# Kernel tuning notes

Hardware: AMD Instinct MI355X
Metric: run time of the kernel (lower is better)

Reference implementation:

```python
import math
import jax, jax.numpy as jnp
import numpy as np

B, T, D = 2, 1024, 768          # batch, seq, hidden
H = 12                          # attention heads
DH_ATT = D // H
PH, NK, TOPK, DHK = 4, 256, 32, 128  # pkm heads, num product keys, topk, key dim
DQ = PH * DHK * 2               # pkm query projection width
EPS = 1e-5


def _ln(x, g, b):
    m = jnp.mean(x, -1, keepdims=True)
    v = jnp.var(x, -1, keepdims=True)
    return (x - m) * jax.lax.rsqrt(v + EPS) * g + b


def setup_inputs() -> dict:
    key = jax.random.key(0)
    k = jax.random.split(key, 8)
    n = lambda i, s, sc=0.02: jax.random.normal(k[i], s, jnp.float32) * sc
    z = lambda s: jnp.zeros(s, jnp.float32)
    o = lambda s: jnp.ones(s, jnp.float32)
    return {
        "hidden_states": jax.random.normal(k[0], (B, T, D), jnp.float32),
        "wq": n(1, (D, D)), "bq": z((D,)),
        "wk": n(2, (D, D)), "bk": z((D,)),
        "wv": n(3, (D, D)), "bv": z((D,)),
        "wo": n(4, (D, D)), "bo": z((D,)),
        "ln1_g": o((D,)), "ln1_b": z((D,)),
        "ln2_g": o((D,)), "ln2_b": z((D,)),
        "pkm_wq": n(5, (D, DQ)),
        "bn_g": o((DQ,)), "bn_b": z((DQ,)),
        "pkm_keys": n(6, (PH, NK, 2, DHK), 1.0 / math.sqrt(DHK)),
        "pkm_values": n(7, (NK * NK, D), 1.0 / math.sqrt(D)),
    }


def reference(hidden_states, wq, bq, wk, bk, wv, bv, wo, bo,
              ln1_g, ln1_b, ln2_g, ln2_b,
              pkm_wq, bn_g, bn_b, pkm_keys, pkm_values):
    x = hidden_states
    # ---- pre-norm self-attention + residual ----
    h = _ln(x, ln1_g, ln1_b)
    q = (h @ wq + bq).reshape(B, T, H, DH_ATT)
    k = (h @ wk + bk).reshape(B, T, H, DH_ATT)
    v = (h @ wv + bv).reshape(B, T, H, DH_ATT)
    scores = jnp.einsum('bqhd,bkhd->bhqk', q, k) / math.sqrt(DH_ATT)
    probs = jax.nn.softmax(scores, axis=-1)
    attn_out = jnp.einsum('bhqk,bkhd->bqhd', probs, v).reshape(B, T, D) @ wo + bo
    x = x + attn_out
    # ---- pre-norm PKM + residual ----
    h = _ln(x, ln2_g, ln2_b)
    qf = (h @ pkm_wq).reshape(B * T, DQ)
    # BatchNorm1d over tokens (training-mode batch stats)
    mu = jnp.mean(qf, 0)
    var = jnp.var(qf, 0)
    qn = (qf - mu) * jax.lax.rsqrt(var + EPS) * bn_g + bn_b
    # split into the two sub-key query halves: [2, n, PH, DHK]
    qh = jnp.stack(jnp.split(qn, 2, axis=-1)).reshape(2, B * T, PH, DHK)
    # distances against both sub-key codebooks: [n, PH, 2, NK]
    dots = jnp.einsum('pnhd,hkpd->nhpk', qh, pkm_keys)
    s, idx = jax.lax.top_k(dots, TOPK)                       # [n, PH, 2, TOPK]
    all_s = (s[:, :, 0, :, None] + s[:, :, 1, None, :]).reshape(B * T, PH, TOPK * TOPK)
    all_i = (idx[:, :, 0, :, None] * NK + idx[:, :, 1, None, :]).reshape(B * T, PH, TOPK * TOPK)
    fs, fpos = jax.lax.top_k(all_s, TOPK)                    # [n, PH, TOPK]
    vi = jnp.take_along_axis(all_i, fpos, axis=-1)           # cartesian indices
    attn = jax.nn.softmax(fs, axis=-1)
    # EmbeddingBag(mode='sum') with per_sample_weights: gather + weighted sum over PH*TOPK
    pkm_out = jnp.einsum('nhk,nhkd->nd', attn, pkm_values[vi]).reshape(B, T, D)
    return x + pkm_out
```

## Files before the change

kernel.cpp:

```cpp
#include <hip/hip_runtime.h>
#include <hip/hip_bf16.h>

#define B_  2
#define T_  1024
#define D_  768
#define H_  12
#define NT  2048
#define DQ_ 1024
#define PH_ 4
#define NK_ 256
#define TK_ 32
#define DHK_ 128
#define QKVLD 2304
#define CVHALF 25165824L
#define NKEYS (PH_ * NK_ * 2 * DHK_)
#define PREPBLKS 3584

typedef __attribute__((ext_vector_type(8))) short bf16x8;
typedef __attribute__((ext_vector_type(4))) float f32x4;
typedef __attribute__((ext_vector_type(2))) float f32x2;

static __device__ __forceinline__ unsigned short f2bf(float f) {
    union { float f; unsigned u; } c; c.f = f;
    unsigned r = (c.u + 0x7fffu + ((c.u >> 16) & 1u)) >> 16;
    return (unsigned short)r;
}

static __device__ __forceinline__ float bf2f(unsigned short s) {
    union { unsigned u; float f; } c; c.u = ((unsigned)s) << 16;
    return c.f;
}

__device__ __constant__ unsigned short ctab[128] = {
    0,1,2,3,4,5,6,7,8,9,10,11,12,13,14,15,16,17,18,19,20,21,22,23,24,25,26,27,28,29,30,31,
    32,33,34,35,36,37,38,39,40,41,42,43,44,45,46,47,
    64,65,66,67,68,69,70,71,72,73,
    96,97,98,99,100,101,102,103,
    128,129,130,131,132,133,
    160,161,162,163,164,
    192,193,194,195,
    224,225,226,227,
    256,257,258,
    288,289,290,
    320,321, 352,353, 384,385, 416,417, 448,449, 480,481,
    512,544,576,608,640,672,704,736,768,800,832,864,896,928,960,992,
    0xFFFF,0xFFFF,0xFFFF,0xFFFF,0xFFFF,0xFFFF,0xFFFF,0xFFFF,0xFFFF
};

__global__ __launch_bounds__(256)
void ln_kernel(const float* __restrict__ x, const float* __restrict__ g,
               const float* __restrict__ b, unsigned short* __restrict__ out,
               int nrows,
               const float* __restrict__ wq, const float* __restrict__ wk,
               const float* __restrict__ wv, const float* __restrict__ wo,
               const float* __restrict__ pwq, const float* __restrict__ keys,
               unsigned short* __restrict__ wqkvT, unsigned short* __restrict__ woT,
               unsigned short* __restrict__ pwqT, unsigned short* __restrict__ keyB) {
    int tid = threadIdx.x;
    if ((int)blockIdx.x >= nrows) {
        int tb = blockIdx.x - nrows;
        if (tb >= 3072) {
            long i = ((long)(tb - 3072) * 256 + tid) * 2;
            if (i + 1 < NKEYS + 1) { keyB[i] = f2bf(keys[i]); keyB[i + 1] = f2bf(keys[i + 1]); }
            return;
        }
        __shared__ float t[32][33];
        const float* W; unsigned short* Wt; int N, kx, ny;
        if (tb < 2304) {
            int z = tb / 576, rem = tb % 576;
            kx = rem % 24; ny = rem / 24; N = 768;
            if (z == 0)      { W = wq; Wt = wqkvT; }
            else if (z == 1) { W = wk; Wt = wqkvT + 589824; }
            else if (z == 2) { W = wv; Wt = wqkvT + 2 * 589824; }
            else             { W = wo; Wt = woT; }
        } else {
            int rem = tb - 2304;
            kx = rem % 24; ny = rem / 24; N = 1024;
            W = pwq; Wt = pwqT;
        }
        int k0 = kx * 32, n0 = ny * 32;
        int tx = tid & 31, ty = tid >> 5;
#pragma unroll
        for (int i = 0; i < 4; ++i)
            t[ty + 8 * i][tx] = W[(long)(k0 + ty + 8 * i) * N + n0 + tx];
        __syncthreads();
#pragma unroll
        for (int i = 0; i < 4; ++i)
            Wt[(long)(n0 + ty + 8 * i) * 768 + k0 + tx] = f2bf(t[tx][ty + 8 * i]);
        return;
    }

    int row = blockIdx.x;
    const float* xr = x + (long)row * D_;
    float v0 = xr[tid], v1 = xr[tid + 256], v2 = xr[tid + 512];
    float s = v0 + v1 + v2, ss = v0 * v0 + v1 * v1 + v2 * v2;
#pragma unroll
    for (int o = 1; o < 64; o <<= 1) { s += __shfl_xor(s, o); ss += __shfl_xor(ss, o); }
    __shared__ float ps[4], pss[4];
    int wid = tid >> 6, lane = tid & 63;
    if (lane == 0) { ps[wid] = s; pss[wid] = ss; }
    __syncthreads();
    s = ps[0] + ps[1] + ps[2] + ps[3];
    ss = pss[0] + pss[1] + pss[2] + pss[3];
    float mean = s * (1.f / D_);
    float var = ss * (1.f / D_) - mean * mean;
    float rs = rsqrtf(var + 1e-5f);
    unsigned short* orow = out + (long)row * D_;
    orow[tid]       = f2bf((v0 - mean) * rs * g[tid]       + b[tid]);
    orow[tid + 256] = f2bf((v1 - mean) * rs * g[tid + 256] + b[tid + 256]);
    orow[tid + 512] = f2bf((v2 - mean) * rs * g[tid + 512] + b[tid + 512]);
}

__global__ __launch_bounds__(256)
void gemm_kernel(const unsigned short* __restrict__ A, int lda,
                 const unsigned short* __restrict__ Bt, int ldb,
                 const float* __restrict__ bias,
                 const float* __restrict__ bias2,
                 const float* __restrict__ bias3,
                 const float* __restrict__ res,
                 float* __restrict__ outF,
                 unsigned short* __restrict__ outB,
                 int ldc, int K, int zmode,
                 const float* __restrict__ cvin,
                 unsigned char* __restrict__ cvout,
                 long cvbase, int cvy0,
                 float* __restrict__ pSo, float* __restrict__ pSSo) {
    if (cvin && (int)blockIdx.y >= cvy0) {
        long stride = (long)(gridDim.y - cvy0) * gridDim.x * 256 * 8;
        long idx = cvbase +
            ((long)((blockIdx.y - cvy0) * gridDim.x + blockIdx.x) * 256 + threadIdx.x) * 8;
        long end = cvbase + CVHALF;
#pragma unroll 2
        for (; idx < end; idx += stride) {
            f32x4 a = *(const f32x4*)(cvin + idx);
            f32x4 b = *(const f32x4*)(cvin + idx + 4);
            int lo = __builtin_amdgcn_cvt_pk_fp8_f32(a[0], a[1], 0, false);
            lo = __builtin_amdgcn_cvt_pk_fp8_f32(a[2], a[3], lo, true);
            int hi = __builtin_amdgcn_cvt_pk_fp8_f32(b[0], b[1], 0, false);
            hi = __builtin_amdgcn_cvt_pk_fp8_f32(b[2], b[3], hi, true);
            *(uint2*)(cvout + idx) = make_uint2((unsigned)lo, (unsigned)hi);
        }
        return;
    }
    const int tid = threadIdx.x;
    const int w = tid >> 6, lane = tid & 63;
    const int ls = lane & 15, g = lane >> 4;
    const int m0 = blockIdx.x * 64, n0 = blockIdx.y * 64;

    __shared__ unsigned short As[64][40];
    __shared__ unsigned short Bs[64][40];

    f32x4 acc[4];
#pragma unroll
    for (int c = 0; c < 4; ++c) acc[c] = (f32x4){0.f, 0.f, 0.f, 0.f};

    const int lrow = tid >> 2, lseg = tid & 3;
    const unsigned short* gA = A + (long)(m0 + lrow) * lda + lseg * 8;
    const unsigned short* gB = Bt + (long)(n0 + lrow) * ldb + lseg * 8;

    for (int kt = 0; kt < K; kt += 32) {
        __syncthreads();
        *(int4*)&As[lrow][lseg * 8] = *(const int4*)(gA + kt);
        *(int4*)&Bs[lrow][lseg * 8] = *(const int4*)(gB + kt);
        __syncthreads();
        bf16x8 bfr = *(const bf16x8*)&Bs[w * 16 + ls][g * 8];
#pragma unroll
        for (int c = 0; c < 4; ++c) {
            bf16x8 afr = *(const bf16x8*)&As[c * 16 + ls][g * 8];
            acc[c] = __builtin_amdgcn_mfma_f32_16x16x32_bf16(afr, bfr, acc[c], 0, 0, 0);
        }
    }
#pragma unroll
    for (int c = 0; c < 4; ++c) {
#pragma unroll
        for (int r = 0; r < 4; ++r) {
            int row = m0 + c * 16 + g * 4 + r;
            int col = n0 + w * 16 + ls;
            float v = acc[c][r];
            if (bias) {
                const float* bp = bias; int cc = col;
                if (zmode == 2) {
                    int sel = col >= 1536 ? 2 : (col >= 768 ? 1 : 0);
                    bp = sel == 0 ? bias : (sel == 1 ? bias2 : bias3);
                    cc = col - sel * 768;
                }
                v += bp[cc];
            }
            long off = (long)row * ldc + col;
            if (res)  v += res[off];
            if (outF) outF[off] = v;
            if (outB) outB[off] = f2bf(v);
        }
    }
    if (pSo) {
        float s = 0.f, ss = 0.f;
#pragma unroll
        for (int c = 0; c < 4; ++c)
#pragma unroll
            for (int r = 0; r < 4; ++r) { float v = acc[c][r]; s += v; ss += v * v; }
        s += __shfl_xor(s, 16); s += __shfl_xor(s, 32);
        ss += __shfl_xor(ss, 16); ss += __shfl_xor(ss, 32);
        if (g == 0) {
            int col = n0 + w * 16 + ls;
            pSo[(long)blockIdx.x * DQ_ + col] = s;
            pSSo[(long)blockIdx.x * DQ_ + col] = ss;
        }
    }
}

__global__ __launch_bounds__(256)
void dots_kernel(const unsigned short* __restrict__ qf,
                 const unsigned short* __restrict__ Bt,
                 const float* __restrict__ pS, const float* __restrict__ pSS,
                 const float* __restrict__ bng, const float* __restrict__ bnb,
                 unsigned short* __restrict__ outB) {
    int z = blockIdx.z, ph = z >> 1, half = z & 1;
    const int cbase = half * 512 + ph * 128;
    const unsigned short* A = qf + cbase;
    Bt   += ph * 65536 + half * 128;
    outB += ph * 512 + half * 256;
    const int tid = threadIdx.x;
    const int w = tid >> 6, lane = tid & 63;
    const int ls = lane & 15, g = lane >> 4;
    const int m0 = blockIdx.x * 64, n0 = blockIdx.y * 64;

    __shared__ unsigned short As[64][136];
    __shared__ unsigned short Bs[64][136];
    __shared__ float ggs[128], bbs[128];

    const int row = tid >> 2, cs = (tid & 3) * 32;
    const unsigned short* gA = A + (long)(m0 + row) * DQ_ + cs;
    const unsigned short* gB = Bt + (long)(n0 + row) * 256 + cs;

    bf16x8 areg[4];
#pragma unroll
    for (int j = 0; j < 4; ++j) {
        areg[j] = *(const bf16x8*)(gA + 8 * j);
        *(int4*)&Bs[row][cs + 8 * j] = *(const int4*)(gB + 8 * j);
    }
    if (tid < 128) {
        int c = cbase + tid;
        float s = 0.f, ss = 0.f;
#pragma unroll 8
        for (int i = 0; i < 32; ++i) { s += pS[(long)i * DQ_ + c]; ss += pSS[(long)i * DQ_ + c]; }
        float m = s * (1.f / NT);
        float rs = rsqrtf(ss * (1.f / NT) - m * m + 1e-5f);
        float gg = bng[c] * rs;
        ggs[tid] = gg;
        bbs[tid] = bnb[c] - m * gg;
    }
    __syncthreads();
#pragma unroll
    for (int j = 0; j < 4; ++j) {
        bf16x8 r;
#pragma unroll
        for (int k = 0; k < 8; ++k) {
            int lc = cs + 8 * j + k;
            r[k] = (short)f2bf(bf2f((unsigned short)areg[j][k]) * ggs[lc] + bbs[lc]);
        }
        *(bf16x8*)&As[row][cs + 8 * j] = r;
    }
    __syncthreads();

    f32x4 acc[4];
#pragma unroll
    for (int c = 0; c < 4; ++c) acc[c] = (f32x4){0.f, 0.f, 0.f, 0.f};
#pragma unroll
    for (int kk = 0; kk < 4; ++kk) {
        bf16x8 bfr = *(const bf16x8*)&Bs[w * 16 + ls][g * 8 + 32 * kk];
#pragma unroll
        for (int c = 0; c < 4; ++c) {
            bf16x8 afr = *(const bf16x8*)&As[c * 16 + ls][g * 8 + 32 * kk];
            acc[c] = __builtin_amdgcn_mfma_f32_16x16x32_bf16(afr, bfr, acc[c], 0, 0, 0);
        }
    }
#pragma unroll
    for (int c = 0; c < 4; ++c)
#pragma unroll
        for (int r = 0; r < 4; ++r)
            outB[(long)(m0 + c * 16 + g * 4 + r) * 2048 + n0 + w * 16 + ls] = f2bf(acc[c][r]);
}

__global__ __launch_bounds__(512)
void attn_mfma_kernel(const unsigned short* __restrict__ qkv,
                      unsigned short* __restrict__ outg) {
    int bh = blockIdx.x, bb = bh / H_, hh = bh % H_;
    int q0 = blockIdx.y * 128;
    int tid = threadIdx.x, wv = tid >> 6, lane = tid & 63;
    int ls = lane & 15, g = lane >> 4;

    __shared__ unsigned short Klds[128 * 64];
    __shared__ unsigned short Vlds[64 * 128];
    __shared__ unsigned short Plds[8][16 * 128];

    const unsigned short* qrow = qkv + (long)(bb * T_ + q0 + wv * 16 + ls) * QKVLD + hh * 64 + g * 8;
    bf16x8 qf0 = *(const bf16x8*)qrow;
    bf16x8 qf1 = *(const bf16x8*)(qrow + 32);

    f32x4 o_acc[4];
#pragma unroll
    for (int nf = 0; nf < 4; ++nf) o_acc[nf] = (f32x4){0.f, 0.f, 0.f, 0.f};
    float mrun[4] = {-1e30f, -1e30f, -1e30f, -1e30f};
    float lrun[4] = {0.f, 0.f, 0.f, 0.f};

    char* pbase = (char*)&Plds[wv][0];
    const bool doK = tid < 256;
    const int t2 = tid & 255;
    const int d0 = (t2 & 7) * 8, kvq = t2 >> 3;

    bf16x8 streg[4];
    auto loadKV = [&](int kvb) {
        if (doK) {
#pragma unroll
            for (int i = 0; i < 4; ++i) {
                int c = t2 + i * 256;
                streg[i] = *(const bf16x8*)(qkv + (long)(bb * T_ + kvb + (c >> 3)) * QKVLD + 768 + hh * 64 + (c & 7) * 8);
            }
        } else {
            const unsigned short* vb = qkv + (long)(bb * T_ + kvb + kvq * 4) * QKVLD + 1536 + hh * 64 + d0;
#pragma unroll
            for (int i = 0; i < 4; ++i) streg[i] = *(const bf16x8*)(vb + i * QKVLD);
        }
    };

    loadKV(0);
    for (int kt = 0; kt < T_ / 128; ++kt) {
        __syncthreads();
        if (doK) {
#pragma unroll
            for (int i = 0; i < 4; ++i) {
                int c = t2 + i * 256;
                int kv = c >> 3, dc = c & 7;
                *(bf16x8*)((char*)Klds + ((kv * 128 + dc * 16) ^ ((kv & 7) << 4))) = streg[i];
            }
        } else {
#pragma unroll
            for (int j = 0; j < 8; ++j) {
                unsigned lo = (unsigned)(unsigned short)streg[0][j] | ((unsigned)(unsigned short)streg[1][j] << 16);
                unsigned hi = (unsigned)(unsigned short)streg[2][j] | ((unsigned)(unsigned short)streg[3][j] << 16);
                int d = d0 + j;
                *(uint2*)((char*)Vlds + ((d * 256 + kvq * 8) ^ ((d & 7) << 4))) = make_uint2(lo, hi);
            }
        }
        __syncthreads();
        if (kt + 1 < T_ / 128) loadKV((kt + 1) * 128);

        f32x4 sa[8];
#pragma unroll
        for (int f = 0; f < 8; ++f) sa[f] = (f32x4){0.f, 0.f, 0.f, 0.f};
        __builtin_amdgcn_s_setprio(1);
#pragma unroll
        for (int f = 0; f < 8; ++f) {
            int kv = f * 16 + ls;
            bf16x8 b0 = *(const bf16x8*)((char*)Klds + ((kv * 128 + g * 16) ^ ((kv & 7) << 4)));
            bf16x8 b1 = *(const bf16x8*)((char*)Klds + ((kv * 128 + 64 + g * 16) ^ ((kv & 7) << 4)));
            sa[f] = __builtin_amdgcn_mfma_f32_16x16x32_bf16(qf0, b0, sa[f], 0, 0, 0);
            sa[f] = __builtin_amdgcn_mfma_f32_16x16x32_bf16(qf1, b1, sa[f], 0, 0, 0);
        }
        __builtin_amdgcn_s_setprio(0);

        float pw[8][4];
#pragma unroll
        for (int f = 0; f < 8; ++f)
#pragma unroll
            for (int r = 0; r < 4; ++r) pw[f][r] = sa[f][r] * 0.125f;
#pragma unroll
        for (int r = 0; r < 4; ++r) {
            float m = pw[0][r];
#pragma unroll
            for (int f = 1; f < 8; ++f) m = fmaxf(m, pw[f][r]);
            m = fmaxf(m, __shfl_xor(m, 1));
            m = fmaxf(m, __shfl_xor(m, 2));
            m = fmaxf(m, __shfl_xor(m, 4));
            m = fmaxf(m, __shfl_xor(m, 8));
            if (m > mrun[r] + 8.f) {
                float fac = __expf(mrun[r] - m);
                lrun[r] *= fac;
#pragma unroll
                for (int nf = 0; nf < 4; ++nf) o_acc[nf][r] *= fac;
                mrun[r] = m;
            }
            float s = 0.f;
#pragma unroll
            for (int f = 0; f < 8; ++f) { float e = __expf(pw[f][r] - mrun[r]); pw[f][r] = e; s += e; }
            s += __shfl_xor(s, 1); s += __shfl_xor(s, 2);
            s += __shfl_xor(s, 4); s += __shfl_xor(s, 8);
            lrun[r] += s;
        }

#pragma unroll
        for (int f = 0; f < 8; ++f)
#pragma unroll
            for (int r = 0; r < 4; ++r) {
                int qr = g * 4 + r, col = ls + 16 * f;
                *(unsigned short*)(pbase + ((qr * 256 + col * 2) ^ ((qr & 7) << 4))) = f2bf(pw[f][r]);
            }

        __builtin_amdgcn_s_setprio(1);
#pragma unroll
        for (int ks = 0; ks < 4; ++ks) {
            bf16x8 pa = *(const bf16x8*)(pbase + ((ls * 256 + ks * 64 + g * 16) ^ ((ls & 7) << 4)));
#pragma unroll
            for (int nf = 0; nf < 4; ++nf) {
                int d = nf * 16 + ls;
                bf16x8 bv = *(const bf16x8*)((char*)Vlds + ((d * 256 + ks * 64 + g * 16) ^ ((d & 7) << 4)));
                o_acc[nf] = __builtin_amdgcn_mfma_f32_16x16x32_bf16(pa, bv, o_acc[nf], 0, 0, 0);
            }
        }
        __builtin_amdgcn_s_setprio(0);
    }

    float inv[4];
#pragma unroll
    for (int r = 0; r < 4; ++r) inv[r] = 1.f / lrun[r];
#pragma unroll
    for (int nf = 0; nf < 4; ++nf)
#pragma unroll
        for (int r = 0; r < 4; ++r) {
            long row = bb * T_ + q0 + wv * 16 + g * 4 + r;
            outg[row * D_ + hh * 64 + nf * 16 + ls] = f2bf(o_acc[nf][r] * inv[r]);
        }
}

__global__ __launch_bounds__(512)
void pkm_tail_fp8(const unsigned short* __restrict__ dots,
                  const unsigned char* __restrict__ vals8,
                  const float* __restrict__ x1,
                  float* __restrict__ outp) {
    __shared__ float sv[4][64];
    __shared__ int   sidx[4][64];
    __shared__ float w[128];
    __shared__ int   rows[128];
    __shared__ float red[3 * 768];
    int n = blockIdx.x, tid = threadIdx.x;
    int wv = tid >> 6, lane = tid & 63;
    int slot = wv >> 1, half = wv & 1;

    {
        const unsigned short* d = dots + (long)n * 2048 + slot * 512 + half * 256;
        float v0 = bf2f(d[lane]), v1 = bf2f(d[lane + 64]);
        float v2 = bf2f(d[lane + 128]), v3 = bf2f(d[lane + 192]);
#pragma unroll 1
        for (int t = 0; t < 32; ++t) {
            float bm = v0; int ba = 0;
            if (v1 > bm) { bm = v1; ba = 1; }
            if (v2 > bm) { bm = v2; ba = 2; }
            if (v3 > bm) { bm = v3; ba = 3; }
            float wm = bm;
#pragma unroll
            for (int o = 32; o >= 1; o >>= 1) wm = fmaxf(wm, __shfl_xor(wm, o));
            unsigned long long msk = __ballot(bm == wm);
            int owner = (int)__builtin_ctzll(msk);
            if (lane == owner) {
                sv[slot][half * 32 + t] = wm;
                sidx[slot][half * 32 + t] = ba * 64 + lane;
                if (ba == 0) v0 = -1e30f;
                else if (ba == 1) v1 = -1e30f;
                else if (ba == 2) v2 = -1e30f;
                else v3 = -1e30f;
            }
        }
    }
    __syncthreads();

    if (!half) {
        unsigned short t0 = ctab[lane], t1 = ctab[lane + 64];
        float c0 = -1e30f, c1 = -1e30f;
        int id0 = 0, id1 = 0;
        {
            int i = t0 >> 5, j = t0 & 31;
            c0 = sv[slot][i] + sv[slot][32 + j];
            id0 = sidx[slot][i] * NK_ + sidx[slot][32 + j];
        }
        if (t1 != 0xFFFF) {
            int i = t1 >> 5, j = t1 & 31;
            c1 = sv[slot][i] + sv[slot][32 + j];
            id1 = sidx[slot][i] * NK_ + sidx[slot][32 + j];
        }
#pragma unroll 1
        for (int t = 0; t < 32; ++t) {
            float bm = c0; int sel = 0;
            if (c1 > bm) { bm = c1; sel = 1; }
            float wm = bm;
#pragma unroll
            for (int o = 32; o >= 1; o >>= 1) wm = fmaxf(wm, __shfl_xor(wm, o));
            unsigned long long msk = __ballot(bm == wm);
            int owner = (int)__builtin_ctzll(msk);
            if (lane == owner) {
                w[slot * 32 + t] = wm;
                rows[slot * 32 + t] = sel ? id1 : id0;
                if (sel) c1 = -1e30f; else c0 = -1e30f;
            }
        }
    }
    __syncthreads();

    if (tid < 128) {
        float e = w[tid];
        float m = e;
#pragma unroll
        for (int o = 16; o >= 1; o >>= 1) m = fmaxf(m, __shfl_xor(m, o));
        float ex = __expf(e - m);
        float s = ex;
#pragma unroll
        for (int o = 16; o >= 1; o >>= 1) s += __shfl_xor(s, o);
        w[tid] = ex / s;
    }
    __syncthreads();

    int gs = tid >> 7, chunk = tid & 127;
    float a0=0.f,a1=0.f,a2=0.f,a3=0.f,a4=0.f,a5=0.f,a6=0.f,a7=0.f;
    if (chunk < 96) {
#pragma unroll 4
        for (int e = 0; e < 32; ++e) {
            int er = e * 4 + gs;
            float wgt = w[er];
            long ro = (long)rows[er] * D_;
            uint2 v = *(const uint2*)(vals8 + ro + chunk * 8);
            f32x2 f0 = __builtin_amdgcn_cvt_pk_f32_fp8((int)v.x, false);
            f32x2 f1 = __builtin_amdgcn_cvt_pk_f32_fp8((int)v.x, true);
            f32x2 f2 = __builtin_amdgcn_cvt_pk_f32_fp8((int)v.y, false);
            f32x2 f3 = __builtin_amdgcn_cvt_pk_f32_fp8((int)v.y, true);
            a0 += wgt * f0[0]; a1 += wgt * f0[1]; a2 += wgt * f1[0]; a3 += wgt * f1[1];
            a4 += wgt * f2[0]; a5 += wgt * f2[1]; a6 += wgt * f3[0]; a7 += wgt * f3[1];
        }
        if (gs > 0) {
            float* rp = &red[(gs - 1) * 768 + chunk * 8];
            rp[0]=a0; rp[1]=a1; rp[2]=a2; rp[3]=a3; rp[4]=a4; rp[5]=a5; rp[6]=a6; rp[7]=a7;
        }
    }
    __syncthreads();
    if (gs == 0 && chunk < 96) {
        long o = (long)n * D_ + chunk * 8;
        const float* r0 = &red[chunk * 8];
        const float* r1 = &red[768 + chunk * 8];
        const float* r2 = &red[1536 + chunk * 8];
        f32x4 xa = *(const f32x4*)(x1 + o);
        f32x4 xb = *(const f32x4*)(x1 + o + 4);
        f32x4 o1 = { a0 + r0[0] + r1[0] + r2[0] + xa[0], a1 + r0[1] + r1[1] + r2[1] + xa[1],
                     a2 + r0[2] + r1[2] + r2[2] + xa[2], a3 + r0[3] + r1[3] + r2[3] + xa[3] };
        f32x4 o2 = { a4 + r0[4] + r1[4] + r2[4] + xb[0], a5 + r0[5] + r1[5] + r2[5] + xb[1],
                     a6 + r0[6] + r1[6] + r2[6] + xb[2], a7 + r0[7] + r1[7] + r2[7] + xb[3] };
        *(f32x4*)(outp + o) = o1;
        *(f32x4*)(outp + o + 4) = o2;
    }
}

__global__ __launch_bounds__(256)
void topk_kernel(const unsigned short* __restrict__ dots, float* __restrict__ fs, int* __restrict__ vi) {
    __shared__ float sv[2][64];
    __shared__ int   sidx[2][64];
    int tid = threadIdx.x, wv = tid >> 6, lane = tid & 63;
    int slot = wv >> 1, half = wv & 1;
    long task = (long)blockIdx.x * 2 + slot;
    const unsigned short* d = dots + (task >> 2) * 2048 + (task & 3) * 512 + half * 256;

    float v0 = bf2f(d[lane]), v1 = bf2f(d[lane + 64]);
    float v2 = bf2f(d[lane + 128]), v3 = bf2f(d[lane + 192]);
#pragma unroll 1
    for (int t = 0; t < 32; ++t) {
        float bm = v0; int ba = 0;
        if (v1 > bm) { bm = v1; ba = 1; }
        if (v2 > bm) { bm = v2; ba = 2; }
        if (v3 > bm) { bm = v3; ba = 3; }
        float wm = bm;
#pragma unroll
        for (int o = 32; o >= 1; o >>= 1) wm = fmaxf(wm, __shfl_xor(wm, o));
        unsigned long long msk = __ballot(bm == wm);
        int owner = (int)__builtin_ctzll(msk);
        if (lane == owner) {
            sv[slot][half * 32 + t] = wm;
            sidx[slot][half * 32 + t] = ba * 64 + lane;
            if (ba == 0) v0 = -1e30f;
            else if (ba == 1) v1 = -1e30f;
            else if (ba == 2) v2 = -1e30f;
            else v3 = -1e30f;
        }
    }
    __syncthreads();
    if (half) return;

    unsigned short t0 = ctab[lane], t1 = ctab[lane + 64];
    float c0 = -1e30f, c1 = -1e30f;
    int id0 = 0, id1 = 0;
    {
        int i = t0 >> 5, j = t0 & 31;
        c0 = sv[slot][i] + sv[slot][32 + j];
        id0 = sidx[slot][i] * NK_ + sidx[slot][32 + j];
    }
    if (t1 != 0xFFFF) {
        int i = t1 >> 5, j = t1 & 31;
        c1 = sv[slot][i] + sv[slot][32 + j];
        id1 = sidx[slot][i] * NK_ + sidx[slot][32 + j];
    }

    float* fo = fs + task * 32;
    int*   vo = vi + task * 32;
#pragma unroll 1
    for (int t = 0; t < 32; ++t) {
        float bm = c0; int sel = 0;
        if (c1 > bm) { bm = c1; sel = 1; }
        float wm = bm;
#pragma unroll
        for (int o = 32; o >= 1; o >>= 1) wm = fmaxf(wm, __shfl_xor(wm, o));
        unsigned long long msk = __ballot(bm == wm);
        int owner = (int)__builtin_ctzll(msk);
        if (lane == owner) {
            fo[t] = wm;
            vo[t] = sel ? id1 : id0;
            if (sel) c1 = -1e30f; else c0 = -1e30f;
        }
    }
}

__global__ __launch_bounds__(384)
void pkm_out_f32(const float* __restrict__ fs, const int* __restrict__ vi,
                 const float* __restrict__ values, const float* __restrict__ x1,
                 float* __restrict__ outp) {
    int n = blockIdx.x, tid = threadIdx.x;
    __shared__ float w[128];
    __shared__ int   rows[128];
    __shared__ float red[768];
    if (tid < 128) {
        float e = fs[(long)n * 128 + tid];
        rows[tid] = vi[(long)n * 128 + tid];
        float m = e;
#pragma unroll
        for (int o = 16; o >= 1; o >>= 1) m = fmaxf(m, __shfl_xor(m, o));
        float ex = __expf(e - m);
        float s = ex;
#pragma unroll
        for (int o = 16; o >= 1; o >>= 1) s += __shfl_xor(s, o);
        w[tid] = ex / s;
    }
    __syncthreads();
    int slot = tid / 192, chunk = tid % 192;
    float a0 = 0.f, a1 = 0.f, a2 = 0.f, a3 = 0.f;
#pragma unroll 4
    for (int e = 0; e < 64; ++e) {
        int er = e * 2 + slot;
        float wgt = w[er];
        long ro = (long)rows[er] * D_;
        f32x4 v = *(const f32x4*)(values + ro + chunk * 4);
        a0 += wgt * v[0]; a1 += wgt * v[1]; a2 += wgt * v[2]; a3 += wgt * v[3];
    }
    if (slot == 1) {
        f32x4 t = {a0, a1, a2, a3};
        *(f32x4*)&red[chunk * 4] = t;
    }
    __syncthreads();
    if (slot == 0) {
        f32x4 o = *(const f32x4*)&red[chunk * 4];
        f32x4 xr = *(const f32x4*)(x1 + (long)n * D_ + chunk * 4);
        o[0] += a0 + xr[0]; o[1] += a1 + xr[1]; o[2] += a2 + xr[2]; o[3] += a3 + xr[3];
        *(f32x4*)(outp + (long)n * D_ + chunk * 4) = o;
    }
}

extern "C" void kernel_launch(void* const* d_in, const int* in_sizes, int n_in,
                              void* d_out, int out_size, void* d_ws, size_t ws_size,
                              hipStream_t stream) {
    const float* x    = (const float*)d_in[0];
    const float* wq   = (const float*)d_in[1];
    const float* bq   = (const float*)d_in[2];
    const float* wk   = (const float*)d_in[3];
    const float* bk   = (const float*)d_in[4];
    const float* wv   = (const float*)d_in[5];
    const float* bv   = (const float*)d_in[6];
    const float* wo   = (const float*)d_in[7];
    const float* bo   = (const float*)d_in[8];
    const float* ln1g = (const float*)d_in[9];
    const float* ln1b = (const float*)d_in[10];
    const float* ln2g = (const float*)d_in[11];
    const float* ln2b = (const float*)d_in[12];
    const float* pwq  = (const float*)d_in[13];
    const float* bng  = (const float*)d_in[14];
    const float* bnb  = (const float*)d_in[15];
    const float* keys = (const float*)d_in[16];
    const float* vals = (const float*)d_in[17];
    float* out = (float*)d_out;

    char* p = (char*)d_ws;
    auto alloc = [&](size_t bytes) -> char* {
        char* r = p; p += (bytes + 255) & ~(size_t)255; return r;
    };
    unsigned short* wqkvT = (unsigned short*)alloc((size_t)3 * D_ * D_ * 2);
    unsigned short* woT   = (unsigned short*)alloc((size_t)D_ * D_ * 2);
    unsigned short* pwqT  = (unsigned short*)alloc((size_t)D_ * DQ_ * 2);
    unsigned short* keyB  = (unsigned short*)alloc((size_t)NKEYS * 2);
    unsigned short* h1    = (unsigned short*)alloc((size_t)NT * D_ * 2);
    unsigned short* qkvB  = (unsigned short*)alloc((size_t)NT * QKVLD * 2);
    unsigned short* aout  = (unsigned short*)alloc((size_t)NT * D_ * 2);
    float* x1             = (float*)alloc((size_t)NT * D_ * 4);
    unsigned short* h2    = (unsigned short*)alloc((size_t)NT * D_ * 2);
    unsigned short* qfB   = (unsigned short*)alloc((size_t)NT * DQ_ * 2);
    float* pS             = (float*)alloc((size_t)32 * DQ_ * 4);
    float* pSS            = (float*)alloc((size_t)32 * DQ_ * 4);
    unsigned short* dots  = (unsigned short*)alloc((size_t)NT * 2048 * 2);
    float* fsb            = (float*)alloc((size_t)NT * PH_ * 32 * 4);
    int*   vib            = (int*)alloc((size_t)NT * PH_ * 32 * 4);

    size_t used = (size_t)(p - (char*)d_ws);
    size_t vbytes = (size_t)NK_ * NK_ * D_;
    bool useTab = (used + vbytes + 256) <= ws_size;
    unsigned char* vals8 = nullptr;
    if (useTab) vals8 = (unsigned char*)alloc(vbytes);

    ln_kernel<<<NT + PREPBLKS, 256, 0, stream>>>(
        x, ln1g, ln1b, h1, NT, wq, wk, wv, wo, pwq, keys, wqkvT, woT, pwqT, keyB);
    gemm_kernel<<<dim3(32, useTab ? 52 : 36), 256, 0, stream>>>(
        h1, D_, wqkvT, D_, bq, bk, bv, nullptr, nullptr, qkvB, QKVLD, D_, 2,
        useTab ? vals : nullptr, vals8, 0L, 36, nullptr, nullptr);
    attn_mfma_kernel<<<dim3(B_ * H_, T_ / 128), 512, 0, stream>>>(qkvB, aout);
    gemm_kernel<<<dim3(32, 12), 256, 0, stream>>>(
        aout, D_, woT, D_, bo, nullptr, nullptr, x, x1, nullptr, D_, D_, 0,
        nullptr, nullptr, 0L, 0, nullptr, nullptr);
    ln_kernel<<<NT, 256, 0, stream>>>(
        x1, ln2g, ln2b, h2, NT, nullptr, nullptr, nullptr, nullptr, nullptr, nullptr,
        nullptr, nullptr, nullptr, nullptr);
    gemm_kernel<<<dim3(32, useTab ? 32 : 16), 256, 0, stream>>>(
        h2, D_, pwqT, D_, nullptr, nullptr, nullptr, nullptr, nullptr, qfB, DQ_, D_, 0,
        useTab ? vals : nullptr, vals8, CVHALF, 16, pS, pSS);
    dots_kernel<<<dim3(32, 4, 8), 256, 0, stream>>>(qfB, keyB, pS, pSS, bng, bnb, dots);
    if (useTab) {
        pkm_tail_fp8<<<NT, 512, 0, stream>>>(dots, vals8, x1, out);
    } else {
        topk_kernel<<<(NT * PH_) / 2, 256, 0, stream>>>(dots, fsb, vib);
        pkm_out_f32<<<NT, 384, 0, stream>>>(fsb, vib, vals, x1, out);
    }
}
```

Measured before the change: 235.6 us.

## Fuse second LayerNorm into output-projection epilogue and PKM query GEMM

The Wo GEMM epilogue now emits per-row partial sums and sums of squares for each column tile. A new PKM query GEMM kernel reduces these into row mean and rstd, applies LayerNorm on the fly while loading fp32 x1 into shared memory as bf16, and also carries the fp8 value-table conversion and the BatchNorm column statistics. This removes the separate LN kernel launch and the h2 round trip through memory. In exchange it reads fp32 activations (twice the bytes of bf16) for every column tile, repeats the normalisation arithmetic in each tile, and computes variance as E[x²]−mean², which loses some numerical precision.

```diff
diff --git a/kernel.cpp b/kernel.cpp
--- a/kernel.cpp
+++ b/kernel.cpp
@@ -124,7 +124,7 @@
                  const float* __restrict__ cvin,
                  unsigned char* __restrict__ cvout,
                  long cvbase, int cvy0,
-                 float* __restrict__ pSo, float* __restrict__ pSSo) {
+                 float* __restrict__ pRo, float* __restrict__ pRRo) {
     if (cvin && (int)blockIdx.y >= cvy0) {
         long stride = (long)(gridDim.y - cvy0) * gridDim.x * 256 * 8;
         long idx = cvbase +
@@ -170,6 +170,7 @@
             acc[c] = __builtin_amdgcn_mfma_f32_16x16x32_bf16(afr, bfr, acc[c], 0, 0, 0);
         }
     }
+    float vv[4][4];
 #pragma unroll
     for (int c = 0; c < 4; ++c) {
 #pragma unroll
@@ -188,23 +189,131 @@
             }
             long off = (long)row * ldc + col;
             if (res)  v += res[off];
+            vv[c][r] = v;
             if (outF) outF[off] = v;
             if (outB) outB[off] = f2bf(v);
         }
     }
-    if (pSo) {
-        float s = 0.f, ss = 0.f;
+    if (pRo) {
+        __shared__ float plsS[4][64], plsQ[4][64];
 #pragma unroll
         for (int c = 0; c < 4; ++c)
 #pragma unroll
-            for (int r = 0; r < 4; ++r) { float v = acc[c][r]; s += v; ss += v * v; }
-        s += __shfl_xor(s, 16); s += __shfl_xor(s, 32);
-        ss += __shfl_xor(ss, 16); ss += __shfl_xor(ss, 32);
-        if (g == 0) {
+            for (int r = 0; r < 4; ++r) {
+                float s = vv[c][r], q = s * s;
+#pragma unroll
+                for (int o = 1; o < 16; o <<= 1) { s += __shfl_xor(s, o); q += __shfl_xor(q, o); }
+                if (ls == 0) { plsS[w][c * 16 + g * 4 + r] = s; plsQ[w][c * 16 + g * 4 + r] = q; }
+            }
+        __syncthreads();
+        if (tid < 64) {
+            float s = plsS[0][tid] + plsS[1][tid] + plsS[2][tid] + plsS[3][tid];
+            float q = plsQ[0][tid] + plsQ[1][tid] + plsQ[2][tid] + plsQ[3][tid];
+            pRo[(long)blockIdx.y * NT + m0 + tid] = s;
+            pRRo[(long)blockIdx.y * NT + m0 + tid] = q;
+        }
+    }
+}
+
+__global__ __launch_bounds__(256)
+void pkmq_kernel(const float* __restrict__ x1,
+                 const unsigned short* __restrict__ Bt,
+                 const float* __restrict__ pR, const float* __restrict__ pRR,
+                 const float* __restrict__ g2, const float* __restrict__ b2,
+                 unsigned short* __restrict__ qfB,
+                 float* __restrict__ pSo, float* __restrict__ pSSo,
+                 const float* __restrict__ cvin, unsigned char* __restrict__ cvout) {
+    if (cvin && (int)blockIdx.y >= 16) {
+        long stride = (long)(gridDim.y - 16) * gridDim.x * 256 * 8;
+        long idx = CVHALF +
+            ((long)((blockIdx.y - 16) * gridDim.x + blockIdx.x) * 256 + threadIdx.x) * 8;
+        long end = 2 * CVHALF;
+#pragma unroll 2
+        for (; idx < end; idx += stride) {
+            f32x4 a = *(const f32x4*)(cvin + idx);
+            f32x4 b = *(const f32x4*)(cvin + idx + 4);
+            int lo = __builtin_amdgcn_cvt_pk_fp8_f32(a[0], a[1], 0, false);
+            lo = __builtin_amdgcn_cvt_pk_fp8_f32(a[2], a[3], lo, true);
+            int hi = __builtin_amdgcn_cvt_pk_fp8_f32(b[0], b[1], 0, false);
+            hi = __builtin_amdgcn_cvt_pk_fp8_f32(b[2], b[3], hi, true);
+            *(uint2*)(cvout + idx) = make_uint2((unsigned)lo, (unsigned)hi);
+        }
+        return;
+    }
+    const int tid = threadIdx.x;
+    const int w = tid >> 6, lane = tid & 63;
+    const int ls = lane & 15, g = lane >> 4;
+    const int m0 = blockIdx.x * 64, n0 = blockIdx.y * 64;
+
+    __shared__ unsigned short As[64][40];
+    __shared__ unsigned short Bs[64][40];
+    __shared__ float rmean[64], rrs[64];
+    __shared__ float g2s[D_], b2s[D_];
+
+    if (tid < 64) {
+        int row = m0 + tid;
+        float s = 0.f, q = 0.f;
+#pragma unroll
+        for (int i = 0; i < 12; ++i) { s += pR[(long)i * NT + row]; q += pRR[(long)i * NT + row]; }
+        float mn = s * (1.f / D_);
+        rmean[tid] = mn;
+        rrs[tid] = rsqrtf(q * (1.f / D_) - mn * mn + 1e-5f);
+    }
+    for (int i = tid; i < D_; i += 256) { g2s[i] = g2[i]; b2s[i] = b2[i]; }
+
+    f32x4 acc[4];
+#pragma unroll
+    for (int c = 0; c < 4; ++c) acc[c] = (f32x4){0.f, 0.f, 0.f, 0.f};
+
+    const int lrow = tid >> 2, lseg = tid & 3;
+    const float* gA = x1 + (long)(m0 + lrow) * D_ + lseg * 8;
+    const unsigned short* gB = Bt + (long)(n0 + lrow) * D_ + lseg * 8;
+
+    for (int kt = 0; kt < D_; kt += 32) {
+        __syncthreads();
+        f32x4 a0 = *(const f32x4*)(gA + kt);
+        f32x4 a1 = *(const f32x4*)(gA + kt + 4);
+        float mn = rmean[lrow], rs = rrs[lrow];
+        bf16x8 r;
+#pragma unroll
+        for (int k = 0; k < 4; ++k) {
+            int col = kt + lseg * 8 + k;
+            r[k] = (short)f2bf((a0[k] - mn) * rs * g2s[col] + b2s[col]);
+        }
+#pragma unroll
+        for (int k = 0; k < 4; ++k) {
+            int col = kt + lseg * 8 + 4 + k;
+            r[4 + k] = (short)f2bf((a1[k] - mn) * rs * g2s[col] + b2s[col]);
+        }
+        *(bf16x8*)&As[lrow][lseg * 8] = r;
+        *(int4*)&Bs[lrow][lseg * 8] = *(const int4*)(gB + kt);
+        __syncthreads();
+        bf16x8 bfr = *(const bf16x8*)&Bs[w * 16 + ls][g * 8];
+#pragma unroll
+        for (int c = 0; c < 4; ++c) {
+            bf16x8 afr = *(const bf16x8*)&As[c * 16 + ls][g * 8];
+            acc[c] = __builtin_amdgcn_mfma_f32_16x16x32_bf16(afr, bfr, acc[c], 0, 0, 0);
+        }
+    }
+#pragma unroll
+    for (int c = 0; c < 4; ++c)
+#pragma unroll
+        for (int r = 0; r < 4; ++r) {
+            int row = m0 + c * 16 + g * 4 + r;
             int col = n0 + w * 16 + ls;
-            pSo[(long)blockIdx.x * DQ_ + col] = s;
-            pSSo[(long)blockIdx.x * DQ_ + col] = ss;
-        }
+            qfB[(long)row * DQ_ + col] = f2bf(acc[c][r]);
+        }
+    float s = 0.f, q = 0.f;
+#pragma unroll
+    for (int c = 0; c < 4; ++c)
+#pragma unroll
+        for (int r = 0; r < 4; ++r) { float v = acc[c][r]; s += v; q += v * v; }
+    s += __shfl_xor(s, 16); s += __shfl_xor(s, 32);
+    q += __shfl_xor(q, 16); q += __shfl_xor(q, 32);
+    if (g == 0) {
+        int col = n0 + w * 16 + ls;
+        pSo[(long)blockIdx.x * DQ_ + col] = s;
+        pSSo[(long)blockIdx.x * DQ_ + col] = q;
     }
 }
 
@@ -692,7 +801,8 @@
     unsigned short* qkvB  = (unsigned short*)alloc((size_t)NT * QKVLD * 2);
     unsigned short* aout  = (unsigned short*)alloc((size_t)NT * D_ * 2);
     float* x1             = (float*)alloc((size_t)NT * D_ * 4);
-    unsigned short* h2    = (unsigned short*)alloc((size_t)NT * D_ * 2);
+    float* pR             = (float*)alloc((size_t)12 * NT * 4);
+    float* pRR            = (float*)alloc((size_t)12 * NT * 4);
     unsigned short* qfB   = (unsigned short*)alloc((size_t)NT * DQ_ * 2);
     float* pS             = (float*)alloc((size_t)32 * DQ_ * 4);
     float* pSS            = (float*)alloc((size_t)32 * DQ_ * 4);
@@ -714,13 +824,10 @@
     attn_mfma_kernel<<<dim3(B_ * H_, T_ / 128), 512, 0, stream>>>(qkvB, aout);
     gemm_kernel<<<dim3(32, 12), 256, 0, stream>>>(
         aout, D_, woT, D_, bo, nullptr, nullptr, x, x1, nullptr, D_, D_, 0,
-        nullptr, nullptr, 0L, 0, nullptr, nullptr);
-    ln_kernel<<<NT, 256, 0, stream>>>(
-        x1, ln2g, ln2b, h2, NT, nullptr, nullptr, nullptr, nullptr, nullptr, nullptr,
-        nullptr, nullptr, nullptr, nullptr);
-    gemm_kernel<<<dim3(32, useTab ? 32 : 16), 256, 0, stream>>>(
-        h2, D_, pwqT, D_, nullptr, nullptr, nullptr, nullptr, nullptr, qfB, DQ_, D_, 0,
-        useTab ? vals : nullptr, vals8, CVHALF, 16, pS, pSS);
+        nullptr, nullptr, 0L, 0, pR, pRR);
+    pkmq_kernel<<<dim3(32, useTab ? 32 : 16), 256, 0, stream>>>(
+        x1, pwqT, pR, pRR, ln2g, ln2b, qfB, pS, pSS,
+        useTab ? vals : nullptr, vals8);
     dots_kernel<<<dim3(32, 4, 8), 256, 0, stream>>>(qfB, keyB, pS, pSS, bng, bnb, dots);
     if (useTab) {
         pkm_tail_fp8<<<NT, 512, 0, stream>>>(dots, vals8, x1, out);
```

After: 238.7 us. No clear change (+1.3%).
